# Optimization experiments

Hardware: AMD Instinct MI355X
Metric: run time of the kernel (lower is better)

Reference implementation:

```python
import jax, jax.numpy as jnp
import numpy as np

B, T, D_V, D_Q = 8, 8192, 1024, 768
K_REP = 6
NUM_HEADS = 8
LN_EPS = 1e-5


def _mlp_ln(x, w1, b1, g, bt, w2, b2):
    # Linear -> LayerNorm -> ReLU -> Linear (torch Linear: y = x @ W.T + b)
    h = x @ w1.T + b1
    m = h.mean(-1, keepdims=True)
    v = ((h - m) ** 2).mean(-1, keepdims=True)
    h = (h - m) / jnp.sqrt(v + LN_EPS) * g + bt
    h = jax.nn.relu(h)
    return h @ w2.T + b2


def _mahalanobis(feat, mu, sigma):
    # feat [B,T,d], mu/sigma [B,d] -> [B,T]
    c = feat - mu[:, None, :]
    return jnp.sum(c * c / sigma[:, None, :], axis=-1)


def _diversify(cand):
    # greedy farthest-point selection on temporal indices; cand [C] int32 -> [K_REP]
    candf = cand.astype(jnp.float32)
    mind = jnp.abs(candf - candf[0]).at[0].set(-jnp.inf)

    def step(mind, _):
        best = jnp.argmax(mind)  # ties -> first remaining, matches np.argmax over ordered list
        sel = cand[best]
        mind = jnp.minimum(mind, jnp.abs(candf - candf[best])).at[best].set(-jnp.inf)
        return mind, sel

    _, rest = jax.lax.scan(step, mind, None, length=K_REP - 1)
    return jnp.concatenate([cand[:1], rest])


def _select_indices(dist):
    # dist [T] -> [K_REP] selected temporal indices
    Tn = dist.shape[0]
    med = jnp.sort(dist)[(Tn - 1) // 2]  # torch.median: lower median
    d2t = jnp.abs(dist - med)
    C = min(K_REP * 3, Tn)
    _, cand = jax.lax.top_k(-d2t, C)  # smallest |d - median|
    return _diversify(cand.astype(jnp.int32))


def _mha(x, in_w, in_b, out_w, out_b):
    # torch nn.MultiheadAttention self-attention, batch_first, averaged attn weights
    b, k, d = x.shape
    hd = d // NUM_HEADS
    qkv = x @ in_w.T + in_b  # [b,k,3d]
    q, kk, v = jnp.split(qkv, 3, axis=-1)
    def heads(t):
        return t.reshape(b, k, NUM_HEADS, hd).transpose(0, 2, 1, 3)  # [b,h,k,hd]
    q, kk, v = heads(q), heads(kk), heads(v)
    scores = jnp.einsum('bhqd,bhkd->bhqk', q, kk) / jnp.sqrt(jnp.asarray(hd, x.dtype))
    attn = jax.nn.softmax(scores, axis=-1)
    out = jnp.einsum('bhqk,bhkd->bhqd', attn, v).transpose(0, 2, 1, 3).reshape(b, k, d)
    out = out @ out_w.T + out_b
    return out, attn.mean(axis=1)  # weights averaged over heads


def setup_inputs() -> dict:
    key = jax.random.key(0)
    ks = jax.random.split(key, 16)
    s = 0.02
    return {
        'video_features': jax.random.normal(ks[0], (B, T, D_V), jnp.float32),
        'query_embedding': jax.random.normal(ks[1], (B, D_Q), jnp.float32),
        'mu_w1': jax.random.normal(ks[2], (D_V, D_Q), jnp.float32) * s,
        'mu_b1': jnp.zeros((D_V,), jnp.float32),
        'mu_g': jnp.ones((D_V,), jnp.float32),
        'mu_bt': jnp.zeros((D_V,), jnp.float32),
        'mu_w2': jax.random.normal(ks[3], (D_V, D_V), jnp.float32) * s,
        'mu_b2': jnp.zeros((D_V,), jnp.float32),
        'sg_w1': jax.random.normal(ks[4], (D_V, D_Q), jnp.float32) * s,
        'sg_b1': jnp.zeros((D_V,), jnp.float32),
        'sg_g': jnp.ones((D_V,), jnp.float32),
        'sg_bt': jnp.zeros((D_V,), jnp.float32),
        'sg_w2': jax.random.normal(ks[5], (D_V, D_V), jnp.float32) * s,
        'sg_b2': jnp.zeros((D_V,), jnp.float32),
        'in_w': jax.random.normal(ks[6], (3 * D_V, D_V), jnp.float32) * s,
        'in_b': jnp.zeros((3 * D_V,), jnp.float32),
        'out_w': jax.random.normal(ks[7], (D_V, D_V), jnp.float32) * s,
        'out_b': jnp.zeros((D_V,), jnp.float32),
    }


def reference(video_features, query_embedding, mu_w1, mu_b1, mu_g, mu_bt, mu_w2, mu_b2,
              sg_w1, sg_b1, sg_g, sg_bt, sg_w2, sg_b2, in_w, in_b, out_w, out_b):
    mu_q = _mlp_ln(query_embedding, mu_w1, mu_b1, mu_g, mu_bt, mu_w2, mu_b2)  # [B,d]
    sigma_q = jax.nn.softplus(_mlp_ln(query_embedding, sg_w1, sg_b1, sg_g, sg_bt, sg_w2, sg_b2)) + 1e-6
    dist = _mahalanobis(video_features, mu_q, sigma_q)  # [B,T]
    idx = jax.vmap(_select_indices)(dist)  # [B,K]
    rep = jax.vmap(lambda f, i: f[i])(video_features, idx)  # gather [B,K,d]
    refined, attn_w = _mha(rep, in_w, in_b, out_w, out_b)
    return refined, idx, dist, mu_q, sigma_q, attn_w
```

## Files before the change

### kernel.cpp

```cpp
#include <hip/hip_runtime.h>
#include <math.h>

#define TNUM 8192
#define BNUM 8
#define DV 1024
#define DQ 768
#define KREP 6
#define NHEAD 8
#define HD 128
#define CANDN 18

__device__ __forceinline__ double wave_reduce_sum(double v) {
    for (int off = 32; off > 0; off >>= 1) v += __shfl_down(v, off);
    return v;
}
__device__ __forceinline__ float wave_reduce_sumf(float v) {
    for (int off = 32; off > 0; off >>= 1) v += __shfl_down(v, off);
    return v;
}

__global__ void k_mlp1(const float* __restrict__ q,
                       const float* __restrict__ mu_w1, const float* __restrict__ mu_b1,
                       const float* __restrict__ sg_w1, const float* __restrict__ sg_b1,
                       double* __restrict__ h) {
    int o = blockIdx.x, b = blockIdx.y, br = blockIdx.z;
    const float* w  = br ? sg_w1 : mu_w1;
    const float* bb = br ? sg_b1 : mu_b1;
    const float* x  = q + (size_t)b * DQ;
    const float* wr = w + (size_t)o * DQ;
    double acc = 0.0;
    for (int j = threadIdx.x; j < DQ; j += 64)
        acc += (double)x[j] * (double)wr[j];
    acc = wave_reduce_sum(acc);
    if (threadIdx.x == 0)
        h[((size_t)br * BNUM + b) * DV + o] = acc + (double)bb[o];
}

__global__ void k_ln(double* __restrict__ h,
                     const float* __restrict__ mg, const float* __restrict__ mbt,
                     const float* __restrict__ sg, const float* __restrict__ sbt) {
    int b = blockIdx.x, br = blockIdx.y;
    const float* g  = br ? sg  : mg;
    const float* bt = br ? sbt : mbt;
    double* row = h + ((size_t)br * BNUM + b) * DV;
    __shared__ double sc[4];
    __shared__ double s_mean, s_rstd;
    int tid = threadIdx.x, wid = tid >> 6, lane = tid & 63;

    double s = 0.0;
    for (int j = tid; j < DV; j += 256) s += row[j];
    s = wave_reduce_sum(s);
    if (lane == 0) sc[wid] = s;
    __syncthreads();
    if (tid == 0) s_mean = (sc[0] + sc[1] + sc[2] + sc[3]) / (double)DV;
    __syncthreads();
    double mean = s_mean;

    double v = 0.0;
    for (int j = tid; j < DV; j += 256) { double c = row[j] - mean; v += c * c; }
    v = wave_reduce_sum(v);
    if (lane == 0) sc[wid] = v;
    __syncthreads();
    if (tid == 0) s_rstd = 1.0 / sqrt((sc[0] + sc[1] + sc[2] + sc[3]) / (double)DV + 1e-5);
    __syncthreads();
    double rstd = s_rstd;

    for (int j = tid; j < DV; j += 256) {
        double val = (row[j] - mean) * rstd * (double)g[j] + (double)bt[j];
        row[j] = val > 0.0 ? val : 0.0;
    }
}

__global__ void k_mlp2(const double* __restrict__ h,
                       const float* __restrict__ mu_w2, const float* __restrict__ mu_b2,
                       const float* __restrict__ sg_w2, const float* __restrict__ sg_b2,
                       double* __restrict__ mu, double* __restrict__ rsig,
                       float* __restrict__ out_mu, float* __restrict__ out_sg) {
    int o = blockIdx.x, b = blockIdx.y, br = blockIdx.z;
    const float* w  = br ? sg_w2 : mu_w2;
    const float* bb = br ? sg_b2 : mu_b2;
    const double* row = h + ((size_t)br * BNUM + b) * DV;
    const float* wr = w + (size_t)o * DV;
    double acc = 0.0;
    for (int j = threadIdx.x; j < DV; j += 64)
        acc += row[j] * (double)wr[j];
    acc = wave_reduce_sum(acc);
    if (threadIdx.x == 0) {
        double v = acc + (double)bb[o];
        if (br == 0) {
            mu[(size_t)b * DV + o] = v;
            out_mu[b * DV + o] = (float)v;
        } else {
            double sp = fmax(v, 0.0) + log1p(exp(-fabs(v)));
            double sig = sp + 1e-6;
            rsig[(size_t)b * DV + o] = 1.0 / sig;
            out_sg[b * DV + o] = (float)sig;
        }
    }
}

__global__ void __launch_bounds__(256) k_dist(
        const float* __restrict__ feat,
        const double* __restrict__ mu, const double* __restrict__ rsig,
        double* __restrict__ distw, float* __restrict__ dist_out) {
    int wid = threadIdx.x >> 6, lane = threadIdx.x & 63;
    int t = blockIdx.x * 4 + wid;
    int b = blockIdx.y;
    const float4* f4 = (const float4*)(feat + ((size_t)b * TNUM + t) * DV);
    const double* m = mu   + (size_t)b * DV;
    const double* r = rsig + (size_t)b * DV;
    double acc = 0.0;
#pragma unroll
    for (int qq = 0; qq < 4; ++qq) {
        int p = lane + 64 * qq;
        float4 f = f4[p];
        int j = p * 4;
        double c0 = (double)f.x - m[j];
        double c1 = (double)f.y - m[j + 1];
        double c2 = (double)f.z - m[j + 2];
        double c3 = (double)f.w - m[j + 3];
        acc += c0 * c0 * r[j] + c1 * c1 * r[j + 1] + c2 * c2 * r[j + 2] + c3 * c3 * r[j + 3];
    }
    acc = wave_reduce_sum(acc);
    if (lane == 0) {
        distw[(size_t)b * TNUM + t] = acc;
        dist_out[b * TNUM + t] = (float)acc;
    }
}

struct SelShared {
    unsigned int hist[256];
    unsigned long long pref;
    int krem;
    unsigned long long kmn[16], kmx[16];
    unsigned long long s_kmin;
    int s_shift;
};

__device__ __forceinline__ unsigned long long raw_key(double v) {
    return (unsigned long long)__double_as_longlong(v);
}

__device__ void block_norm_params(const double* sw, int absmode, double med,
                                  SelShared* S, int tid) {
    unsigned long long mn = ~0ULL, mx = 0ULL;
    for (int i = tid; i < TNUM; i += 1024) {
        double v = sw[i];
        if (absmode) v = fabs(v - med);
        unsigned long long k = raw_key(v);
        mn = mn < k ? mn : k;
        mx = mx > k ? mx : k;
    }
    for (int off = 32; off > 0; off >>= 1) {
        unsigned long long omn = __shfl_down(mn, off);
        unsigned long long omx = __shfl_down(mx, off);
        mn = mn < omn ? mn : omn;
        mx = mx > omx ? mx : omx;
    }
    int lane = tid & 63, wid = tid >> 6;
    if (lane == 0) { S->kmn[wid] = mn; S->kmx[wid] = mx; }
    __syncthreads();
    if (tid == 0) {
        unsigned long long fmn = S->kmn[0], fmx = S->kmx[0];
        for (int k = 1; k < 16; ++k) {
            if (S->kmn[k] < fmn) fmn = S->kmn[k];
            if (S->kmx[k] > fmx) fmx = S->kmx[k];
        }
        unsigned long long diff = fmx - fmn;
        S->s_kmin = fmn;
        S->s_shift = diff ? __clzll((long long)diff) : 0;
    }
    __syncthreads();
}

__device__ __forceinline__ unsigned long long norm_key(double v, int absmode, double med,
                                                       unsigned long long kmin, int shift) {
    unsigned long long k = raw_key(absmode ? fabs(v - med) : v);
    return (k - kmin) << shift;
}

__device__ unsigned long long block_radix_select(
        const double* sw, int rank, int absmode, double med, SelShared* S, int tid) {
    unsigned long long kmin = S->s_kmin;
    int shift = S->s_shift;
    if (tid == 0) { S->pref = 0ULL; S->krem = rank; }
    __syncthreads();
    for (int p = 0; p < 8; ++p) {
        for (int cc = tid; cc < 256; cc += 1024) S->hist[cc] = 0;
        __syncthreads();
        unsigned long long pref = S->pref;
        int known = 8 * p;
        int sh = 56 - known;
        for (int i = tid; i < TNUM; i += 1024) {
            unsigned long long key = norm_key(sw[i], absmode, med, kmin, shift);
            bool ok = (known == 0) || ((key >> (64 - known)) == (pref >> (64 - known)));
            if (ok) atomicAdd(&S->hist[(unsigned)((key >> sh) & 255ULL)], 1u);
        }
        __syncthreads();
        if (tid < 64) {
            unsigned int s0 = S->hist[tid * 4] + S->hist[tid * 4 + 1] +
                              S->hist[tid * 4 + 2] + S->hist[tid * 4 + 3];
            unsigned int incl = s0;
            for (int off = 1; off < 64; off <<= 1) {
                unsigned int v = __shfl_up(incl, off);
                if (tid >= off) incl += v;
            }
            int krem = S->krem;
            unsigned long long msk = __ballot(incl > (unsigned int)krem);
            int fl = __ffsll((unsigned long long)msk) - 1;
            if (tid == fl) {
                int k = krem - (int)(incl - s0);
                int c = tid * 4;
                while (k >= (int)S->hist[c]) { k -= (int)S->hist[c]; ++c; }
                S->krem = k;
                S->pref = pref | ((unsigned long long)(unsigned)c << sh);
            }
        }
        __syncthreads();
    }
    return S->pref;
}

__global__ void __launch_bounds__(1024) k_select(
        const double* __restrict__ distw,
        float* __restrict__ idx_out, int* __restrict__ idx_int) {
    __shared__ double sw[TNUM];
    __shared__ SelShared S;
    __shared__ int s_cntlt, s_cnteq, s_nlt;
    __shared__ int s_lt[32];
    __shared__ int s_eq[64];
    __shared__ int s_eqs[CANDN];
    __shared__ int s_cand[CANDN];
    int b = blockIdx.x, tid = threadIdx.x;
    const double* w = distw + (size_t)b * TNUM;
    for (int i = tid; i < TNUM; i += 1024) sw[i] = w[i];
    __syncthreads();

    block_norm_params(sw, 0, 0.0, &S, tid);
    unsigned long long kmin1 = S.s_kmin; int shift1 = S.s_shift;
    unsigned long long mk = block_radix_select(sw, (TNUM - 1) / 2, 0, 0.0, &S, tid);
    double med = __longlong_as_double((long long)((mk >> shift1) + kmin1));
    __syncthreads();

    block_norm_params(sw, 1, med, &S, tid);
    unsigned long long kmin2 = S.s_kmin; int shift2 = S.s_shift;
    unsigned long long K = block_radix_select(sw, CANDN - 1, 1, med, &S, tid);

    if (tid == 0) { s_cntlt = 0; s_cnteq = 0; }
    __syncthreads();
    for (int i = tid; i < TNUM; i += 1024) {
        unsigned long long key = norm_key(sw[i], 1, med, kmin2, shift2);
        if (key < K) { int p = atomicAdd(&s_cntlt, 1); if (p < 32) s_lt[p] = i; }
        else if (key == K) { int p = atomicAdd(&s_cnteq, 1); if (p < 64) s_eq[p] = i; }
    }
    __syncthreads();

    if (tid < 64) {
        int nlt = s_cntlt; if (nlt > CANDN - 1) nlt = CANDN - 1;
        int neq = s_cnteq; if (neq > 64) neq = 64;
        int need = CANDN - nlt;
        int mye = (tid < neq) ? s_eq[tid] : 0x7FFFFFFF;
        int r = 0;
        for (int j = 0; j < neq; ++j) { int oj = __shfl(mye, j); if (oj < mye) ++r; }
        if (tid < neq && r < need) s_eqs[r] = mye;
        if (tid == 0) s_nlt = nlt;
    }
    __syncthreads();

    if (tid < 64) {
        int nlt = s_nlt;
        unsigned long long mykey; int myidx;
        if (tid < nlt) {
            myidx = s_lt[tid];
            mykey = norm_key(sw[myidx], 1, med, kmin2, shift2);
        } else if (tid < CANDN) {
            myidx = s_eqs[tid - nlt];
            mykey = K;
        } else { myidx = 0x7FFFFFFF; mykey = ~0ULL; }
        int r = 0;
        for (int j = 0; j < CANDN; ++j) {
            unsigned long long kj = __shfl(mykey, j);
            int ij = __shfl(myidx, j);
            if (kj < mykey || (kj == mykey && ij < myidx)) ++r;
        }
        if (tid < CANDN) s_cand[r] = myidx;
    }
    __syncthreads();

    if (tid < 64) {
        int ci = (tid < CANDN) ? s_cand[tid] : 0;
        float cf = (float)ci;
        float c0 = __shfl(cf, 0);
        const float NEG = -__builtin_huge_valf();
        float mind = (tid < CANDN) ? fabsf(cf - c0) : NEG;
        if (tid == 0) {
            mind = NEG;
            idx_out[b * KREP] = (float)ci;
            idx_int[b * KREP] = ci;
        }
        for (int s = 1; s < KREP; ++s) {
            float bv = mind; int bl = tid;
            for (int off = 32; off > 0; off >>= 1) {
                float ov = __shfl_down(bv, off);
                int   ol = __shfl_down(bl, off);
                if (ov > bv || (ov == bv && ol < bl)) { bv = ov; bl = ol; }
            }
            int bestlane = __shfl(bl, 0);
            float bf = __shfl(cf, bestlane);
            int   bi = __shfl(ci, bestlane);
            if (tid == 0) {
                idx_out[b * KREP + s] = (float)bi;
                idx_int[b * KREP + s] = bi;
            }
            mind = fminf(mind, fabsf(cf - bf));
            if (tid == bestlane) mind = NEG;
        }
    }
}

__global__ void __launch_bounds__(256) k_qkv(
        const float* __restrict__ feat, const int* __restrict__ idxi,
        const float* __restrict__ in_w, const float* __restrict__ in_b,
        float* __restrict__ qkv) {
    int wid = threadIdx.x >> 6, lane = threadIdx.x & 63;
    int o0 = blockIdx.x * 4;
    const float4* w4 = (const float4*)in_w;
    float4 wr[4][4];
#pragma unroll
    for (int rr = 0; rr < 4; ++rr)
#pragma unroll
        for (int qq = 0; qq < 4; ++qq)
            wr[rr][qq] = w4[(size_t)(o0 + rr) * 256 + lane + 64 * qq];
#pragma unroll
    for (int tt = 0; tt < 12; ++tt) {
        int tok = wid + 4 * tt;
        int b = tok / KREP;
        int t = idxi[tok];
        const float4* f4 = (const float4*)(feat + ((size_t)b * TNUM + t) * DV);
        float4 fq[4];
#pragma unroll
        for (int qq = 0; qq < 4; ++qq) fq[qq] = f4[lane + 64 * qq];
        float a0 = 0.f, a1 = 0.f, a2 = 0.f, a3 = 0.f;
#pragma unroll
        for (int qq = 0; qq < 4; ++qq) {
            float4 f = fq[qq];
            a0 += f.x * wr[0][qq].x + f.y * wr[0][qq].y + f.z * wr[0][qq].z + f.w * wr[0][qq].w;
            a1 += f.x * wr[1][qq].x + f.y * wr[1][qq].y + f.z * wr[1][qq].z + f.w * wr[1][qq].w;
            a2 += f.x * wr[2][qq].x + f.y * wr[2][qq].y + f.z * wr[2][qq].z + f.w * wr[2][qq].w;
            a3 += f.x * wr[3][qq].x + f.y * wr[3][qq].y + f.z * wr[3][qq].z + f.w * wr[3][qq].w;
        }
        a0 = wave_reduce_sumf(a0);
        a1 = wave_reduce_sumf(a1);
        a2 = wave_reduce_sumf(a2);
        a3 = wave_reduce_sumf(a3);
        if (lane == 0) {
            float* dst = qkv + (size_t)tok * (3 * DV) + o0;
            dst[0] = a0 + in_b[o0];
            dst[1] = a1 + in_b[o0 + 1];
            dst[2] = a2 + in_b[o0 + 2];
            dst[3] = a3 + in_b[o0 + 3];
        }
    }
}

__global__ void k_attn(const float* __restrict__ qkv,
                       float* __restrict__ attn_h, float* __restrict__ ctx) {
    int h = blockIdx.x, b = blockIdx.y;
    __shared__ float sq[KREP * HD], sk[KREP * HD], sv[KREP * HD];
    __shared__ float sat[KREP * KREP];
    int tid = threadIdx.x;
    for (int p = tid; p < KREP * HD; p += 64) {
        int i = p >> 7, d = p & 127;
        size_t base = (size_t)(b * KREP + i) * (3 * DV) + h * HD + d;
        sq[p] = qkv[base];
        sk[p] = qkv[base + DV];
        sv[p] = qkv[base + 2 * DV];
    }
    __syncthreads();
    if (tid < KREP * KREP) {
        int i = tid / KREP, j = tid % KREP;
        float s = 0.0f;
        for (int d = 0; d < HD; ++d) s += sq[i * HD + d] * sk[j * HD + d];
        sat[tid] = s / sqrtf((float)HD);
    }
    __syncthreads();
    if (tid < KREP) {
        float m = sat[tid * KREP];
        for (int j = 1; j < KREP; ++j) m = fmaxf(m, sat[tid * KREP + j]);
        float sum = 0.0f;
        for (int j = 0; j < KREP; ++j) {
            float e = expf(sat[tid * KREP + j] - m);
            sum += e; sat[tid * KREP + j] = e;
        }
        float inv = 1.0f / sum;
        for (int j = 0; j < KREP; ++j) sat[tid * KREP + j] *= inv;
    }
    __syncthreads();
    if (tid < KREP * KREP)
        attn_h[(size_t)(b * NHEAD + h) * (KREP * KREP) + tid] = sat[tid];
    for (int p = tid; p < KREP * HD; p += 64) {
        int i = p >> 7, d = p & 127;
        float acc = 0.0f;
        for (int j = 0; j < KREP; ++j) acc += sat[i * KREP + j] * sv[j * HD + d];
        ctx[(size_t)(b * KREP + i) * DV + h * HD + d] = acc;
    }
}

__global__ void __launch_bounds__(256) k_proj(
        const float* __restrict__ ctx,
        const float* __restrict__ out_w, const float* __restrict__ out_b,
        float* __restrict__ refined) {
    int wid = threadIdx.x >> 6, lane = threadIdx.x & 63;
    int o0 = blockIdx.x * 4;
    const float4* w4 = (const float4*)out_w;
    float4 wr[4][4];
#pragma unroll
    for (int rr = 0; rr < 4; ++rr)
#pragma unroll
        for (int qq = 0; qq < 4; ++qq)
            wr[rr][qq] = w4[(size_t)(o0 + rr) * 256 + lane + 64 * qq];
#pragma unroll
    for (int tt = 0; tt < 12; ++tt) {
        int tok = wid + 4 * tt;
        const float4* f4 = (const float4*)(ctx + (size_t)tok * DV);
        float4 fq[4];
#pragma unroll
        for (int qq = 0; qq < 4; ++qq) fq[qq] = f4[lane + 64 * qq];
        float a0 = 0.f, a1 = 0.f, a2 = 0.f, a3 = 0.f;
#pragma unroll
        for (int qq = 0; qq < 4; ++qq) {
            float4 f = fq[qq];
            a0 += f.x * wr[0][qq].x + f.y * wr[0][qq].y + f.z * wr[0][qq].z + f.w * wr[0][qq].w;
            a1 += f.x * wr[1][qq].x + f.y * wr[1][qq].y + f.z * wr[1][qq].z + f.w * wr[1][qq].w;
            a2 += f.x * wr[2][qq].x + f.y * wr[2][qq].y + f.z * wr[2][qq].z + f.w * wr[2][qq].w;
            a3 += f.x * wr[3][qq].x + f.y * wr[3][qq].y + f.z * wr[3][qq].z + f.w * wr[3][qq].w;
        }
        a0 = wave_reduce_sumf(a0);
        a1 = wave_reduce_sumf(a1);
        a2 = wave_reduce_sumf(a2);
        a3 = wave_reduce_sumf(a3);
        if (lane == 0) {
            float* dst = refined + (size_t)tok * DV + o0;
            dst[0] = a0 + out_b[o0];
            dst[1] = a1 + out_b[o0 + 1];
            dst[2] = a2 + out_b[o0 + 2];
            dst[3] = a3 + out_b[o0 + 3];
        }
    }
}

__global__ void k_attnmean(const float* __restrict__ attn_h, float* __restrict__ out) {
    int e = threadIdx.x;
    if (e >= BNUM * KREP * KREP) return;
    int b = e / (KREP * KREP), r = e % (KREP * KREP);
    float s = 0.0f;
    for (int h = 0; h < NHEAD; ++h)
        s += attn_h[(size_t)(b * NHEAD + h) * (KREP * KREP) + r];
    out[e] = s * (1.0f / NHEAD);
}

extern "C" void kernel_launch(void* const* d_in, const int* in_sizes, int n_in,
                              void* d_out, int out_size, void* d_ws, size_t ws_size,
                              hipStream_t stream) {
    const float* feat  = (const float*)d_in[0];
    const float* query = (const float*)d_in[1];
    const float* mu_w1 = (const float*)d_in[2];
    const float* mu_b1 = (const float*)d_in[3];
    const float* mu_g  = (const float*)d_in[4];
    const float* mu_bt = (const float*)d_in[5];
    const float* mu_w2 = (const float*)d_in[6];
    const float* mu_b2 = (const float*)d_in[7];
    const float* sg_w1 = (const float*)d_in[8];
    const float* sg_b1 = (const float*)d_in[9];
    const float* sg_g  = (const float*)d_in[10];
    const float* sg_bt = (const float*)d_in[11];
    const float* sg_w2 = (const float*)d_in[12];
    const float* sg_b2 = (const float*)d_in[13];
    const float* in_w  = (const float*)d_in[14];
    const float* in_b  = (const float*)d_in[15];
    const float* out_w = (const float*)d_in[16];
    const float* out_b = (const float*)d_in[17];

    float* out = (float*)d_out;
    float* out_refined = out;
    float* out_idx     = out + 49152;
    float* out_dist    = out + 49200;
    float* out_mu      = out + 114736;
    float* out_sg      = out + 122928;
    float* out_attn    = out + 131120;

    char* ws = (char*)d_ws;
    size_t off = 0;
    auto alloc = [&](size_t bytes) -> void* {
        void* p = (void*)(ws + off);
        off += (bytes + 255) & ~(size_t)255;
        return p;
    };
    double* h      = (double*)alloc((size_t)2 * BNUM * DV * sizeof(double));
    double* muw    = (double*)alloc((size_t)BNUM * DV * sizeof(double));
    double* rsig   = (double*)alloc((size_t)BNUM * DV * sizeof(double));
    double* distw  = (double*)alloc((size_t)BNUM * TNUM * sizeof(double));
    int*    idxi   = (int*)   alloc((size_t)BNUM * KREP * sizeof(int));
    float*  qkv    = (float*) alloc((size_t)BNUM * KREP * 3 * DV * sizeof(float));
    float*  attn_h = (float*) alloc((size_t)BNUM * NHEAD * KREP * KREP * sizeof(float));
    float*  ctx    = (float*) alloc((size_t)BNUM * KREP * DV * sizeof(float));

    k_mlp1<<<dim3(DV, BNUM, 2), 64, 0, stream>>>(query, mu_w1, mu_b1, sg_w1, sg_b1, h);
    k_ln  <<<dim3(BNUM, 2), 256, 0, stream>>>(h, mu_g, mu_bt, sg_g, sg_bt);
    k_mlp2<<<dim3(DV, BNUM, 2), 64, 0, stream>>>(h, mu_w2, mu_b2, sg_w2, sg_b2,
                                                 muw, rsig, out_mu, out_sg);
    k_dist<<<dim3(TNUM / 4, BNUM), 256, 0, stream>>>(feat, muw, rsig, distw, out_dist);
    k_select<<<dim3(BNUM), 1024, 0, stream>>>(distw, out_idx, idxi);
    k_qkv<<<dim3(3 * DV / 4), 256, 0, stream>>>(feat, idxi, in_w, in_b, qkv);
    k_attn<<<dim3(NHEAD, BNUM), 64, 0, stream>>>(qkv, attn_h, ctx);
    k_proj<<<dim3(DV / 4), 256, 0, stream>>>(ctx, out_w, out_b, out_refined);
    k_attnmean<<<dim3(1), 320, 0, stream>>>(attn_h, out_attn);
}
```

Baseline: 515.3 us.

## Reuse mu/rsig registers across rows in k_dist; fuse head-mean into attention kernel

k_dist now processes 32 timesteps per block. Each lane loads its mu and 1/sigma slice into registers once and reuses them across 8 rows, so repeated global loads of the double vectors go away and the grid gets smaller. The attention kernel now runs one block per batch, with one wave per head and padded shared memory. It computes the head-averaged attention weights in the same kernel, which removes the k_attnmean launch and the intermediate buffer. The trade-offs are 32 double registers per lane in k_dist, fewer blocks in flight, and only 8 blocks for the attention step.

```diff
diff --git a/kernel.cpp b/kernel.cpp
--- a/kernel.cpp
+++ b/kernel.cpp
@@ -9,6 +9,7 @@
 #define NHEAD 8
 #define HD 128
 #define CANDN 18
+#define APAD 132
 
 __device__ __forceinline__ double wave_reduce_sum(double v) {
     for (int off = 32; off > 0; off >>= 1) v += __shfl_down(v, off);
@@ -104,27 +105,37 @@
         const double* __restrict__ mu, const double* __restrict__ rsig,
         double* __restrict__ distw, float* __restrict__ dist_out) {
     int wid = threadIdx.x >> 6, lane = threadIdx.x & 63;
-    int t = blockIdx.x * 4 + wid;
     int b = blockIdx.y;
-    const float4* f4 = (const float4*)(feat + ((size_t)b * TNUM + t) * DV);
+    int t0 = blockIdx.x * 32;
     const double* m = mu   + (size_t)b * DV;
     const double* r = rsig + (size_t)b * DV;
-    double acc = 0.0;
+    double md[4][4], rd[4][4];
 #pragma unroll
     for (int qq = 0; qq < 4; ++qq) {
-        int p = lane + 64 * qq;
-        float4 f = f4[p];
-        int j = p * 4;
-        double c0 = (double)f.x - m[j];
-        double c1 = (double)f.y - m[j + 1];
-        double c2 = (double)f.z - m[j + 2];
-        double c3 = (double)f.w - m[j + 3];
-        acc += c0 * c0 * r[j] + c1 * c1 * r[j + 1] + c2 * c2 * r[j + 2] + c3 * c3 * r[j + 3];
-    }
-    acc = wave_reduce_sum(acc);
-    if (lane == 0) {
-        distw[(size_t)b * TNUM + t] = acc;
-        dist_out[b * TNUM + t] = (float)acc;
+        int j = (lane + 64 * qq) * 4;
+#pragma unroll
+        for (int e = 0; e < 4; ++e) { md[qq][e] = m[j + e]; rd[qq][e] = r[j + e]; }
+    }
+#pragma unroll 2
+    for (int rr = 0; rr < 8; ++rr) {
+        int t = t0 + rr * 4 + wid;
+        const float4* f4 = (const float4*)(feat + ((size_t)b * TNUM + t) * DV);
+        double acc = 0.0;
+#pragma unroll
+        for (int qq = 0; qq < 4; ++qq) {
+            float4 f = f4[lane + 64 * qq];
+            double c0 = (double)f.x - md[qq][0];
+            double c1 = (double)f.y - md[qq][1];
+            double c2 = (double)f.z - md[qq][2];
+            double c3 = (double)f.w - md[qq][3];
+            acc += c0 * c0 * rd[qq][0] + c1 * c1 * rd[qq][1]
+                 + c2 * c2 * rd[qq][2] + c3 * c3 * rd[qq][3];
+        }
+        acc = wave_reduce_sum(acc);
+        if (lane == 0) {
+            distw[(size_t)b * TNUM + t] = acc;
+            dist_out[b * TNUM + t] = (float)acc;
+        }
     }
 }
 
@@ -363,46 +374,59 @@
     }
 }
 
-__global__ void k_attn(const float* __restrict__ qkv,
-                       float* __restrict__ attn_h, float* __restrict__ ctx) {
-    int h = blockIdx.x, b = blockIdx.y;
-    __shared__ float sq[KREP * HD], sk[KREP * HD], sv[KREP * HD];
-    __shared__ float sat[KREP * KREP];
-    int tid = threadIdx.x;
-    for (int p = tid; p < KREP * HD; p += 64) {
+__global__ void __launch_bounds__(512) k_attn(
+        const float* __restrict__ qkv,
+        float* __restrict__ ctx, float* __restrict__ out_attn) {
+    int b = blockIdx.x;
+    int tid = threadIdx.x, h = tid >> 6, lane = tid & 63;
+    __shared__ float sq[NHEAD][KREP * APAD];
+    __shared__ float sk[NHEAD][KREP * APAD];
+    __shared__ float sv[NHEAD][KREP * APAD];
+    __shared__ float sat[NHEAD][KREP * KREP];
+
+    for (int p = lane; p < KREP * HD; p += 64) {
         int i = p >> 7, d = p & 127;
         size_t base = (size_t)(b * KREP + i) * (3 * DV) + h * HD + d;
-        sq[p] = qkv[base];
-        sk[p] = qkv[base + DV];
-        sv[p] = qkv[base + 2 * DV];
-    }
-    __syncthreads();
-    if (tid < KREP * KREP) {
-        int i = tid / KREP, j = tid % KREP;
+        sq[h][i * APAD + d] = qkv[base];
+        sk[h][i * APAD + d] = qkv[base + DV];
+        sv[h][i * APAD + d] = qkv[base + 2 * DV];
+    }
+    __syncthreads();
+
+    if (lane < KREP * KREP) {
+        int i = lane / KREP, j = lane % KREP;
         float s = 0.0f;
-        for (int d = 0; d < HD; ++d) s += sq[i * HD + d] * sk[j * HD + d];
-        sat[tid] = s / sqrtf((float)HD);
-    }
-    __syncthreads();
-    if (tid < KREP) {
-        float m = sat[tid * KREP];
-        for (int j = 1; j < KREP; ++j) m = fmaxf(m, sat[tid * KREP + j]);
+        for (int d = 0; d < HD; ++d)
+            s += sq[h][i * APAD + d] * sk[h][j * APAD + d];
+        sat[h][lane] = s / sqrtf((float)HD);
+    }
+    __syncthreads();
+
+    if (lane < KREP) {
+        int i = lane;
+        float m = sat[h][i * KREP];
+        for (int j = 1; j < KREP; ++j) m = fmaxf(m, sat[h][i * KREP + j]);
         float sum = 0.0f;
         for (int j = 0; j < KREP; ++j) {
-            float e = expf(sat[tid * KREP + j] - m);
-            sum += e; sat[tid * KREP + j] = e;
+            float e = expf(sat[h][i * KREP + j] - m);
+            sum += e; sat[h][i * KREP + j] = e;
         }
         float inv = 1.0f / sum;
-        for (int j = 0; j < KREP; ++j) sat[tid * KREP + j] *= inv;
-    }
-    __syncthreads();
-    if (tid < KREP * KREP)
-        attn_h[(size_t)(b * NHEAD + h) * (KREP * KREP) + tid] = sat[tid];
-    for (int p = tid; p < KREP * HD; p += 64) {
+        for (int j = 0; j < KREP; ++j) sat[h][i * KREP + j] *= inv;
+    }
+    __syncthreads();
+
+    for (int p = lane; p < KREP * HD; p += 64) {
         int i = p >> 7, d = p & 127;
         float acc = 0.0f;
-        for (int j = 0; j < KREP; ++j) acc += sat[i * KREP + j] * sv[j * HD + d];
+        for (int j = 0; j < KREP; ++j)
+            acc += sat[h][i * KREP + j] * sv[h][j * APAD + d];
         ctx[(size_t)(b * KREP + i) * DV + h * HD + d] = acc;
+    }
+    if (tid < KREP * KREP) {
+        float s = 0.0f;
+        for (int hh = 0; hh < NHEAD; ++hh) s += sat[hh][tid];
+        out_attn[b * KREP * KREP + tid] = s * (1.0f / NHEAD);
     }
 }
 
@@ -447,16 +471,6 @@
             dst[3] = a3 + out_b[o0 + 3];
         }
     }
-}
-
-__global__ void k_attnmean(const float* __restrict__ attn_h, float* __restrict__ out) {
-    int e = threadIdx.x;
-    if (e >= BNUM * KREP * KREP) return;
-    int b = e / (KREP * KREP), r = e % (KREP * KREP);
-    float s = 0.0f;
-    for (int h = 0; h < NHEAD; ++h)
-        s += attn_h[(size_t)(b * NHEAD + h) * (KREP * KREP) + r];
-    out[e] = s * (1.0f / NHEAD);
 }
 
 extern "C" void kernel_launch(void* const* d_in, const int* in_sizes, int n_in,
@@ -502,17 +516,15 @@
     double* distw  = (double*)alloc((size_t)BNUM * TNUM * sizeof(double));
     int*    idxi   = (int*)   alloc((size_t)BNUM * KREP * sizeof(int));
     float*  qkv    = (float*) alloc((size_t)BNUM * KREP * 3 * DV * sizeof(float));
-    float*  attn_h = (float*) alloc((size_t)BNUM * NHEAD * KREP * KREP * sizeof(float));
     float*  ctx    = (float*) alloc((size_t)BNUM * KREP * DV * sizeof(float));
 
     k_mlp1<<<dim3(DV, BNUM, 2), 64, 0, stream>>>(query, mu_w1, mu_b1, sg_w1, sg_b1, h);
     k_ln  <<<dim3(BNUM, 2), 256, 0, stream>>>(h, mu_g, mu_bt, sg_g, sg_bt);
     k_mlp2<<<dim3(DV, BNUM, 2), 64, 0, stream>>>(h, mu_w2, mu_b2, sg_w2, sg_b2,
                                                  muw, rsig, out_mu, out_sg);
-    k_dist<<<dim3(TNUM / 4, BNUM), 256, 0, stream>>>(feat, muw, rsig, distw, out_dist);
+    k_dist<<<dim3(TNUM / 32, BNUM), 256, 0, stream>>>(feat, muw, rsig, distw, out_dist);
     k_select<<<dim3(BNUM), 1024, 0, stream>>>(distw, out_idx, idxi);
     k_qkv<<<dim3(3 * DV / 4), 256, 0, stream>>>(feat, idxi, in_w, in_b, qkv);
-    k_attn<<<dim3(NHEAD, BNUM), 64, 0, stream>>>(qkv, attn_h, ctx);
+    k_attn<<<dim3(BNUM), 512, 0, stream>>>(qkv, ctx, out_attn);
     k_proj<<<dim3(DV / 4), 256, 0, stream>>>(ctx, out_w, out_b, out_refined);
-    k_attnmean<<<dim3(1), 320, 0, stream>>>(attn_h, out_attn);
-}
+}
```

New measurement: 519.0 us. Within noise of the previous version (+0.7%).
